# Performance work log

Hardware: AMD Instinct MI355X
Metric: run time of the kernel (lower is better)

## Reference

```python
import jax, jax.numpy as jnp
import numpy as np

N_NODES = 100000
N_EDGES = 3200000
F_IN = 16


def gcn_conv(x, edge_index, W, b):
    """PyG GCNConv: x' = D^{-1/2} (A + I) D^{-1/2} (x W) + b,
    with degree computed after adding self-loops."""
    n = x.shape[0]
    xw = x @ W  # [N, F_out]
    row, col = edge_index[0], edge_index[1]  # messages flow row -> col
    ones = jnp.ones(row.shape, dtype=x.dtype)
    deg = jax.ops.segment_sum(ones, col, num_segments=n) + 1.0  # +1 for self-loop
    dinv = jax.lax.rsqrt(deg)  # [N]
    norm = dinv[row] * dinv[col]  # [E]
    msg = xw[row] * norm[:, None]  # [E, F_out]
    out = jax.ops.segment_sum(msg, col, num_segments=n)
    out = out + xw * (1.0 / deg)[:, None]  # self-loop term: norm = 1/deg
    return out + b


def setup_inputs() -> dict:
    key = jax.random.key(0)
    ks = jax.random.split(key, 8)
    x = jax.random.normal(ks[0], (N_NODES, F_IN), dtype=jnp.float32)
    edge_index = jax.random.randint(ks[1], (2, N_EDGES), 0, N_NODES, dtype=jnp.int32)
    # GCNConv weights (glorot in PyG; random normal scaled for the reference)
    W1 = jax.random.normal(ks[2], (F_IN, 4), dtype=jnp.float32) * 0.3
    W2 = jax.random.normal(ks[3], (4, 2), dtype=jnp.float32) * 0.5
    W3 = jax.random.normal(ks[4], (2, 1), dtype=jnp.float32) * 0.7
    b1 = jnp.zeros((4,), jnp.float32)
    b2 = jnp.zeros((2,), jnp.float32)
    b3 = jnp.zeros((1,), jnp.float32)
    return {"x": x, "edge_index": edge_index, "W1": W1, "b1": b1,
            "W2": W2, "b2": b2, "W3": W3, "b3": b3}


def reference(x, edge_index, W1, b1, W2, b2, W3, b3):
    # encode(): GCNConv -> relu -> GCNConv -> relu -> GCNConv -> tanh
    # (dropout is identity in eval mode)
    h = jax.nn.relu(gcn_conv(x, edge_index, W1, b1))
    h = jax.nn.relu(gcn_conv(h, edge_index, W2, b2))
    return jnp.tanh(gcn_conv(h, edge_index, W3, b3))  # [N, 1]
```

## Files before the change

### kernel.cpp

```cpp
#include <hip/hip_runtime.h>
#include <math.h>


static constexpr int BSHIFT = 7;
static constexpr int BCOLS  = 128;
static constexpr int NBMAX  = 1024;
static constexpr int CAP    = 5120;
static constexpr int PAD    = 16;
static constexpr int PBLK   = 512;
static constexpr int PITER  = 16;
static constexpr int PCHUNK = PBLK * PITER;
static constexpr int SBLK   = 512;
static constexpr int GBLK   = 512;

__global__ __launch_bounds__(PBLK) void partition_kernel(
        const int* __restrict__ row, const int* __restrict__ col,
        int* __restrict__ cnt, unsigned int* __restrict__ part,
        int e, int nbuck) {
    __shared__ unsigned int   staged[PCHUNK];
    __shared__ unsigned short bkid[PCHUNK];
    __shared__ int hist[NBMAX];
    __shared__ int excl[NBMAX];
    __shared__ int gbase[NBMAX];
    __shared__ int wsum[8];
    const int t = (int)threadIdx.x;
    for (int j = t; j < NBMAX; j += PBLK) hist[j] = 0;
    __syncthreads();

    const int blockstart = blockIdx.x * PCHUNK;
    const int m = min(PCHUNK, e - blockstart);

    unsigned int pay[PITER];
    unsigned int meta[PITER];
#pragma unroll
    for (int i = 0; i < PITER; ++i) {
        int idx = blockstart + i * PBLK + t;
        if (idx < e) {
            int c = col[idx], r = row[idx];
            int bk = c >> BSHIFT;
            pay[i] = ((unsigned int)(c & (BCOLS - 1)) << 17) | (unsigned int)r;
            int rnk = atomicAdd(&hist[bk], 1);
            meta[i] = ((unsigned int)bk << 13) | (unsigned int)rnk;
        } else {
            meta[i] = 0xFFFFFFFFu;
        }
    }
    __syncthreads();

    int a0 = hist[2 * t], a1 = hist[2 * t + 1];
    int pairsum = a0 + a1;
    int incl = pairsum;
#pragma unroll
    for (int d = 1; d < 64; d <<= 1) {
        int v = __shfl_up(incl, d, 64);
        if ((t & 63) >= d) incl += v;
    }
    int wid = t >> 6, lane = t & 63;
    if (lane == 63) wsum[wid] = incl;
    __syncthreads();
    int woff = 0;
#pragma unroll
    for (int w = 0; w < 8; ++w)
        woff += (w < wid) ? wsum[w] : 0;
    int exclPair = woff + incl - pairsum;
    excl[2 * t]     = exclPair;
    excl[2 * t + 1] = exclPair + a0;
    for (int j = t; j < nbuck; j += PBLK) {
        int h = hist[j];
        gbase[j] = h ? atomicAdd(&cnt[j * PAD], h) : 0;
    }
    __syncthreads();

#pragma unroll
    for (int i = 0; i < PITER; ++i) {
        if (meta[i] != 0xFFFFFFFFu) {
            int bk  = (int)(meta[i] >> 13);
            int rnk = (int)(meta[i] & 0x1FFFu);
            int pos = excl[bk] + rnk;
            staged[pos] = pay[i];
            bkid[pos]   = (unsigned short)bk;
        }
    }
    __syncthreads();

    for (int k = t; k < m; k += PBLK) {
        int bk  = bkid[k];
        int off2 = gbase[bk] + (k - excl[bk]);
        if (off2 < CAP)
            part[(size_t)bk * CAP + off2] = staged[k];
    }
}

__global__ __launch_bounds__(SBLK) void sort_y1_kernel(
        unsigned int* __restrict__ part, const int* __restrict__ cnt,
        const float* __restrict__ x, const float* __restrict__ W1,
        int* __restrict__ rs, int* __restrict__ re, float* __restrict__ dinv,
        float* __restrict__ y1, int n) {
    __shared__ unsigned int   staged[CAP];
    __shared__ unsigned int   sorted[CAP];
    __shared__ unsigned short srank[CAP];
    __shared__ int hist[BCOLS];
    __shared__ int scanb[BCOLS];
    const int b = blockIdx.x;
    const int m = min(cnt[b * PAD], CAP);
    const size_t segbase = (size_t)b * CAP;

    if (threadIdx.x < BCOLS) hist[threadIdx.x] = 0;
    __syncthreads();
    for (int k = threadIdx.x; k < m; k += SBLK) {
        unsigned int v = part[segbase + k];
        staged[k] = v;
        srank[k] = (unsigned short)atomicAdd(&hist[v >> 17], 1);
    }
    __syncthreads();

    if (threadIdx.x < BCOLS) scanb[threadIdx.x] = hist[threadIdx.x];
    __syncthreads();
    for (int off = 1; off < BCOLS; off <<= 1) {
        int v = 0;
        if (threadIdx.x < BCOLS && (int)threadIdx.x >= off)
            v = scanb[threadIdx.x - off];
        __syncthreads();
        if (threadIdx.x < BCOLS) scanb[threadIdx.x] += v;
        __syncthreads();
    }

    for (int k = threadIdx.x; k < m; k += SBLK) {
        unsigned int v = staged[k];
        int lc = (int)(v >> 17);
        sorted[(scanb[lc] - hist[lc]) + (int)srank[k]] = v & 0x1FFFFu;
    }
    __syncthreads();

    for (int k = threadIdx.x; k < m; k += SBLK)
        part[segbase + k] = sorted[k];

    int lc = (int)threadIdx.x >> 2;
    int f  = (int)threadIdx.x & 3;
    int node = b * BCOLS + lc;
    if (node < n) {
        int deg = hist[lc];
        float di = rsqrtf((float)(deg + 1));
        if (f == 0) {
            int start = (int)segbase + (scanb[lc] - deg);
            rs[node] = start;
            re[node] = start + deg;
            dinv[node] = di;
        }
        const float4* x4 = (const float4*)x + (size_t)node * 4;
        float4 r0 = x4[0], r1 = x4[1], r2 = x4[2], r3 = x4[3];
        float a = 0.0f;
        a = fmaf(r0.x, W1[0 * 4 + f], a);  a = fmaf(r0.y, W1[1 * 4 + f], a);
        a = fmaf(r0.z, W1[2 * 4 + f], a);  a = fmaf(r0.w, W1[3 * 4 + f], a);
        a = fmaf(r1.x, W1[4 * 4 + f], a);  a = fmaf(r1.y, W1[5 * 4 + f], a);
        a = fmaf(r1.z, W1[6 * 4 + f], a);  a = fmaf(r1.w, W1[7 * 4 + f], a);
        a = fmaf(r2.x, W1[8 * 4 + f], a);  a = fmaf(r2.y, W1[9 * 4 + f], a);
        a = fmaf(r2.z, W1[10 * 4 + f], a); a = fmaf(r2.w, W1[11 * 4 + f], a);
        a = fmaf(r3.x, W1[12 * 4 + f], a); a = fmaf(r3.y, W1[13 * 4 + f], a);
        a = fmaf(r3.z, W1[14 * 4 + f], a); a = fmaf(r3.w, W1[15 * 4 + f], a);
        y1[node * 4 + f] = a * di;
    }
}

template <int F, int FN, int ACT, int SUBW>
__global__ __launch_bounds__(GBLK) void gather_kernel(
        const int* __restrict__ rs, const int* __restrict__ re,
        const unsigned int* __restrict__ csr,
        const float* __restrict__ y, const float* __restrict__ dinv,
        const float* __restrict__ bias, const float* __restrict__ Wn,
        float* __restrict__ outv, int n) {
    int t = blockIdx.x * GBLK + (int)threadIdx.x;
    int node = t / SUBW;
    int lane = t % SUBW;
    if (node >= n) return;
    int s = rs[node], tend = re[node];
    float acc[F];
#pragma unroll
    for (int f = 0; f < F; ++f) acc[f] = 0.0f;
    const float4* y4 = (const float4*)y;
    const float2* y2p = (const float2*)y;
    int k = s + lane;
    for (; k + SUBW < tend; k += 2 * SUBW) {
        int r0 = (int)csr[k];
        int r1 = (int)csr[k + SUBW];
        if constexpr (F == 4) {
            float4 a0 = y4[r0];
            float4 a1 = y4[r1];
            acc[0] += a0.x + a1.x; acc[1] += a0.y + a1.y;
            acc[2] += a0.z + a1.z; acc[3] += a0.w + a1.w;
        } else if constexpr (F == 2) {
            float2 a0 = y2p[r0];
            float2 a1 = y2p[r1];
            acc[0] += a0.x + a1.x; acc[1] += a0.y + a1.y;
        } else {
            acc[0] += y[r0] + y[r1];
        }
    }
    if (k < tend) {
        int r0 = (int)csr[k];
        if constexpr (F == 4) {
            float4 a0 = y4[r0];
            acc[0] += a0.x; acc[1] += a0.y; acc[2] += a0.z; acc[3] += a0.w;
        } else if constexpr (F == 2) {
            float2 a0 = y2p[r0];
            acc[0] += a0.x; acc[1] += a0.y;
        } else {
            acc[0] += y[r0];
        }
    }
#pragma unroll
    for (int off = SUBW / 2; off > 0; off >>= 1)
#pragma unroll
        for (int f = 0; f < F; ++f) acc[f] += __shfl_xor(acc[f], off);
    if (lane == 0) {
        float di = dinv[node];
        float h[F];
#pragma unroll
        for (int f = 0; f < F; ++f) {
            float z = di * (acc[f] + y[node * F + f]) + bias[f];
            if (ACT == 1) z = fmaxf(z, 0.0f);
            if (ACT == 2) z = tanhf(z);
            h[f] = z;
        }
        if constexpr (FN > 0) {
            float o[FN];
#pragma unroll
            for (int g = 0; g < FN; ++g) o[g] = 0.0f;
#pragma unroll
            for (int f = 0; f < F; ++f)
#pragma unroll
                for (int g = 0; g < FN; ++g)
                    o[g] = fmaf(h[f], Wn[f * FN + g], o[g]);
#pragma unroll
            for (int g = 0; g < FN; ++g) outv[node * FN + g] = o[g] * di;
        } else {
#pragma unroll
            for (int f = 0; f < F; ++f) outv[node * F + f] = h[f];
        }
    }
}

extern "C" void kernel_launch(void* const* d_in, const int* in_sizes, int n_in,
                              void* d_out, int out_size, void* d_ws, size_t ws_size,
                              hipStream_t stream) {
    const float* x  = (const float*)d_in[0];
    const int*   ei = (const int*)d_in[1];
    const float* W1 = (const float*)d_in[2];
    const float* b1 = (const float*)d_in[3];
    const float* W2 = (const float*)d_in[4];
    const float* b2 = (const float*)d_in[5];
    const float* W3 = (const float*)d_in[6];
    const float* b3 = (const float*)d_in[7];
    float* out = (float*)d_out;

    const int n = in_sizes[0] / 16;
    const int e = in_sizes[1] / 2;
    const int* row = ei;
    const int* col = ei + e;

    const int nbuck = (n + BCOLS - 1) / BCOLS;

    size_t off = 0;
    auto take = [&](size_t cnt_) {
        char* p = (char*)d_ws + off * 4;
        off += (cnt_ + 15) & ~(size_t)15;
        return p;
    };
    int* cnt           = (int*)take((size_t)nbuck * PAD);
    unsigned int* part = (unsigned int*)take((size_t)nbuck * CAP);
    int* rs            = (int*)take(n);
    int* re            = (int*)take(n);
    float* dinv        = (float*)take(n);
    float* y1          = (float*)take(4 * n);
    float* y2          = (float*)take(2 * n);
    float* y3          = (float*)take(n);

    hipMemsetAsync(cnt, 0, (size_t)nbuck * PAD * sizeof(int), stream);

    const int pnb = (e + PCHUNK - 1) / PCHUNK;
    partition_kernel<<<pnb, PBLK, 0, stream>>>(row, col, cnt, part, e, nbuck);

    sort_y1_kernel<<<nbuck, SBLK, 0, stream>>>(part, cnt, x, W1, rs, re, dinv, y1, n);

    {
        const int gg = (n * 16 + GBLK - 1) / GBLK;
        gather_kernel<4, 2, 1, 16><<<gg, GBLK, 0, stream>>>(rs, re, part, y1, dinv, b1, W2, y2, n);
    }
    {
        const int gg = (n * 8 + GBLK - 1) / GBLK;
        gather_kernel<2, 1, 1, 8><<<gg, GBLK, 0, stream>>>(rs, re, part, y2, dinv, b2, W3, y3, n);
    }
    {
        const int gg = (n * 8 + GBLK - 1) / GBLK;
        gather_kernel<1, 0, 2, 8><<<gg, GBLK, 0, stream>>>(rs, re, part, y3, dinv, b3, nullptr, out, n);
    }
}
```

Measured before the change: 109.7 us.

## Privatize shared-memory histograms per wave group to cut atomic contention

The partition kernel now runs 1024-thread blocks with 10 items per thread and splits its bucket histogram into two copies chosen by wave parity. The stable offset of each copy is folded into the final scatter position. The per-block sort kernel likewise keeps four histogram copies, with prefix offsets per copy per column. Both changes aim to reduce contention on LDS atomics during counting, at the cost of extra LDS, a larger partition block, and more complex offset arithmetic.

```diff
diff --git a/kernel.cpp b/kernel.cpp
--- a/kernel.cpp
+++ b/kernel.cpp
@@ -7,8 +7,8 @@
 static constexpr int NBMAX  = 1024;
 static constexpr int CAP    = 5120;
 static constexpr int PAD    = 16;
-static constexpr int PBLK   = 512;
-static constexpr int PITER  = 16;
+static constexpr int PBLK   = 1024;
+static constexpr int PITER  = 10;
 static constexpr int PCHUNK = PBLK * PITER;
 static constexpr int SBLK   = 512;
 static constexpr int GBLK   = 512;
@@ -19,16 +19,20 @@
         int e, int nbuck) {
     __shared__ unsigned int   staged[PCHUNK];
     __shared__ unsigned short bkid[PCHUNK];
-    __shared__ int hist[NBMAX];
+    __shared__ int hist0[NBMAX];
+    __shared__ int hist1[NBMAX];
     __shared__ int excl[NBMAX];
     __shared__ int gbase[NBMAX];
-    __shared__ int wsum[8];
+    __shared__ int wsum[16];
     const int t = (int)threadIdx.x;
-    for (int j = t; j < NBMAX; j += PBLK) hist[j] = 0;
+    hist0[t] = 0;
+    hist1[t] = 0;
     __syncthreads();
 
     const int blockstart = blockIdx.x * PCHUNK;
     const int m = min(PCHUNK, e - blockstart);
+    const int copy = (t >> 6) & 1;
+    int* myhist = copy ? hist1 : hist0;
 
     unsigned int pay[PITER];
     unsigned int meta[PITER];
@@ -39,17 +43,17 @@
             int c = col[idx], r = row[idx];
             int bk = c >> BSHIFT;
             pay[i] = ((unsigned int)(c & (BCOLS - 1)) << 17) | (unsigned int)r;
-            int rnk = atomicAdd(&hist[bk], 1);
-            meta[i] = ((unsigned int)bk << 13) | (unsigned int)rnk;
+            int rnk = atomicAdd(&myhist[bk], 1);
+            meta[i] = ((unsigned int)bk << 14) | (unsigned int)rnk;
         } else {
             meta[i] = 0xFFFFFFFFu;
         }
     }
     __syncthreads();
 
-    int a0 = hist[2 * t], a1 = hist[2 * t + 1];
-    int pairsum = a0 + a1;
-    int incl = pairsum;
+    int h0 = hist0[t], h1 = hist1[t];
+    int tot = h0 + h1;
+    int incl = tot;
 #pragma unroll
     for (int d = 1; d < 64; d <<= 1) {
         int v = __shfl_up(incl, d, 64);
@@ -60,23 +64,18 @@
     __syncthreads();
     int woff = 0;
 #pragma unroll
-    for (int w = 0; w < 8; ++w)
+    for (int w = 0; w < 16; ++w)
         woff += (w < wid) ? wsum[w] : 0;
-    int exclPair = woff + incl - pairsum;
-    excl[2 * t]     = exclPair;
-    excl[2 * t + 1] = exclPair + a0;
-    for (int j = t; j < nbuck; j += PBLK) {
-        int h = hist[j];
-        gbase[j] = h ? atomicAdd(&cnt[j * PAD], h) : 0;
-    }
+    excl[t] = woff + incl - tot;
+    gbase[t] = tot ? atomicAdd(&cnt[t * PAD], tot) : 0;
     __syncthreads();
 
 #pragma unroll
     for (int i = 0; i < PITER; ++i) {
         if (meta[i] != 0xFFFFFFFFu) {
-            int bk  = (int)(meta[i] >> 13);
-            int rnk = (int)(meta[i] & 0x1FFFu);
-            int pos = excl[bk] + rnk;
+            int bk  = (int)(meta[i] >> 14);
+            int rnk = (int)(meta[i] & 0x3FFFu);
+            int pos = excl[bk] + (copy ? hist0[bk] : 0) + rnk;
             staged[pos] = pay[i];
             bkid[pos]   = (unsigned short)bk;
         }
@@ -97,49 +96,60 @@
         int* __restrict__ rs, int* __restrict__ re, float* __restrict__ dinv,
         float* __restrict__ y1, int n) {
     __shared__ unsigned int   staged[CAP];
-    __shared__ unsigned int   sorted[CAP];
+    __shared__ unsigned int   sorted_[CAP];
     __shared__ unsigned short srank[CAP];
-    __shared__ int hist[BCOLS];
+    __shared__ int hist[4][BCOLS];
+    __shared__ int coff[4][BCOLS];
     __shared__ int scanb[BCOLS];
     const int b = blockIdx.x;
+    const int t = (int)threadIdx.x;
     const int m = min(cnt[b * PAD], CAP);
     const size_t segbase = (size_t)b * CAP;
-
-    if (threadIdx.x < BCOLS) hist[threadIdx.x] = 0;
-    __syncthreads();
-    for (int k = threadIdx.x; k < m; k += SBLK) {
+    const int copy = (t >> 6) & 3;
+
+    for (int j = t; j < 4 * BCOLS; j += SBLK) (&hist[0][0])[j] = 0;
+    __syncthreads();
+    for (int k = t; k < m; k += SBLK) {
         unsigned int v = part[segbase + k];
         staged[k] = v;
-        srank[k] = (unsigned short)atomicAdd(&hist[v >> 17], 1);
-    }
-    __syncthreads();
-
-    if (threadIdx.x < BCOLS) scanb[threadIdx.x] = hist[threadIdx.x];
+        srank[k] = (unsigned short)atomicAdd(&hist[copy][v >> 17], 1);
+    }
+    __syncthreads();
+
+    if (t < BCOLS) {
+        int h0 = hist[0][t], h1 = hist[1][t], h2 = hist[2][t];
+        coff[0][t] = 0;
+        coff[1][t] = h0;
+        coff[2][t] = h0 + h1;
+        coff[3][t] = h0 + h1 + h2;
+        scanb[t]   = coff[3][t] + hist[3][t];
+    }
     __syncthreads();
     for (int off = 1; off < BCOLS; off <<= 1) {
         int v = 0;
-        if (threadIdx.x < BCOLS && (int)threadIdx.x >= off)
-            v = scanb[threadIdx.x - off];
+        if (t < BCOLS && t >= off) v = scanb[t - off];
         __syncthreads();
-        if (threadIdx.x < BCOLS) scanb[threadIdx.x] += v;
+        if (t < BCOLS) scanb[t] += v;
         __syncthreads();
     }
 
-    for (int k = threadIdx.x; k < m; k += SBLK) {
+    for (int k = t; k < m; k += SBLK) {
         unsigned int v = staged[k];
         int lc = (int)(v >> 17);
-        sorted[(scanb[lc] - hist[lc]) + (int)srank[k]] = v & 0x1FFFFu;
-    }
-    __syncthreads();
-
-    for (int k = threadIdx.x; k < m; k += SBLK)
-        part[segbase + k] = sorted[k];
-
-    int lc = (int)threadIdx.x >> 2;
-    int f  = (int)threadIdx.x & 3;
+        int deg = coff[3][lc] + hist[3][lc];
+        int startpos = scanb[lc] - deg;
+        sorted_[startpos + coff[copy][lc] + (int)srank[k]] = v & 0x1FFFFu;
+    }
+    __syncthreads();
+
+    for (int k = t; k < m; k += SBLK)
+        part[segbase + k] = sorted_[k];
+
+    int lc = t >> 2;
+    int f  = t & 3;
     int node = b * BCOLS + lc;
     if (node < n) {
-        int deg = hist[lc];
+        int deg = coff[3][lc] + hist[3][lc];
         float di = rsqrtf((float)(deg + 1));
         if (f == 0) {
             int start = (int)segbase + (scanb[lc] - deg);
```

After: 107.8 us. No clear change (-1.8%).
